# Kernel tuning notes

Measured on AMD Instinct MI355X. Metric: run time of the kernel, lower is better.

Reference implementation:

```python
import jax, jax.numpy as jnp
import numpy as np

G, N, F, H, E = 3, 40000, 256, 128, 640000


def gcn_conv(x, W, b, edge_index):
    """PyG GCNConv: x @ W, add self-loops, sym-normalized scatter-add, + bias."""
    n = x.shape[0]
    x = x @ W
    loop = jnp.arange(n)
    row = jnp.concatenate([edge_index[0], loop])  # source nodes
    col = jnp.concatenate([edge_index[1], loop])  # target nodes
    deg = jax.ops.segment_sum(jnp.ones_like(row, dtype=x.dtype), col, num_segments=n)
    dinv = jnp.where(deg > 0, jax.lax.rsqrt(jnp.maximum(deg, 1e-12)), 0.0)
    norm = dinv[row] * dinv[col]
    out = jax.ops.segment_sum(x[row] * norm[:, None], col, num_segments=n)
    return out + b


def setup_inputs() -> dict:
    key = jax.random.key(0)
    ks = jax.random.split(key, 14)
    inp = {
        'x': jax.random.normal(ks[0], (G, N, F), jnp.float32),
        'edge_index': jax.random.randint(ks[1], (G, 2, E), 0, N, jnp.int64),
        'fc1_W': jax.random.normal(ks[2], (G, F, H), jnp.float32) * 0.05,
        'fc1_b': jax.random.normal(ks[3], (G, H), jnp.float32) * 0.05,
        'conv1_W': jax.random.normal(ks[4], (G, H, H), jnp.float32) * 0.05,
        'conv1_b': jax.random.normal(ks[5], (G, H), jnp.float32) * 0.05,
        'conv2_W': jax.random.normal(ks[6], (G, H, H), jnp.float32) * 0.05,
        'conv2_b': jax.random.normal(ks[7], (G, H), jnp.float32) * 0.05,
        'dconv1_W': jax.random.normal(ks[8], (G, H, H), jnp.float32) * 0.05,
        'dconv1_b': jax.random.normal(ks[9], (G, H), jnp.float32) * 0.05,
        'dconv2_W': jax.random.normal(ks[10], (G, H, H), jnp.float32) * 0.05,
        'dconv2_b': jax.random.normal(ks[11], (G, H), jnp.float32) * 0.05,
        'fc2_W': jax.random.normal(ks[12], (H, F), jnp.float32) * 0.05,
        'fc2_b': jax.random.normal(ks[13], (F,), jnp.float32) * 0.05,
    }
    return inp


def reference(x, edge_index, fc1_W, fc1_b, conv1_W, conv1_b, conv2_W, conv2_b,
              dconv1_W, dconv1_b, dconv2_W, dconv2_b, fc2_W, fc2_b):
    def encoder(xi, ei, fw, fb, c1w, c1b, c2w, c2b):
        pre = xi @ fw + fb                     # fc1
        h = gcn_conv(pre, c1w, c1b, ei)
        h = gcn_conv(h, c2w, c2b, ei)
        return pre, jax.nn.relu(h)

    pre_feat, enc = jax.vmap(encoder)(x, edge_index, fc1_W, fc1_b,
                                      conv1_W, conv1_b, conv2_W, conv2_b)

    # Faithful reproduction of the sequentially-mutating cross-graph block.
    h = [enc[i] for i in range(G)]
    for i in range(G):
        for j in range(G):
            if j != i:
                h[i] = h[i] + h[j]
        h[i] = h[G - 1] - h[i]  # loop var j ends at G-1 (zeroes tensor when i==G-1)
        h[i] = gcn_conv(h[i], dconv1_W[i], dconv1_b[i], edge_index[i])
        h[i] = gcn_conv(h[i], dconv2_W[i], dconv2_b[i], edge_index[i])

    fin_feat = h[0]
    for k in range(1, G - 1):
        fin_feat = fin_feat + h[k]

    loss_embedding = jax.nn.softmax(fin_feat @ fc2_W + fc2_b, axis=-1)
    return pre_feat, enc, jnp.stack(h), fin_feat, loss_embedding
```

## Files before the change

kernel.cpp:

```cpp
#include <hip/hip_runtime.h>
#include <hip/hip_bf16.h>

#define NV 40000
#define FD 256
#define HD 128
#define ED 640000
#define NG 3
#define NH (NV*HD)

#define CH  64
#define EPC (ED/CH)
#define NB  625

typedef unsigned short u16;
typedef unsigned int   u32;
typedef __attribute__((ext_vector_type(8))) u16    u16x8;
typedef __attribute__((ext_vector_type(8))) __bf16 bf16x8;
typedef __attribute__((ext_vector_type(4))) float  f32x4;

__device__ inline u16 f2b(float f){ __bf16 h = (__bf16)f; return __builtin_bit_cast(u16, h); }
__device__ inline float b2f(u16 u){ u32 x = ((u32)u)<<16; return __builtin_bit_cast(float, x); }

__global__ __launch_bounds__(256) void histB_k(const int* __restrict__ ei, int* __restrict__ btot){
  int ch=blockIdx.x, g=blockIdx.y, t=threadIdx.x;
  __shared__ int h[NB];
  for (int i=t;i<NB;i+=256) h[i]=0;
  __syncthreads();
  const int* cc = ei + (long)g*2*ED + ED + ch*EPC;
  for (int j=t;j<EPC;j+=256) atomicAdd(&h[cc[j]>>6],1);
  __syncthreads();
  for (int b=t;b<NB;b+=256){ int v=h[b]; if(v) atomicAdd(&btot[g*NB+b], v); }
}

__global__ void scanB_k(const int* __restrict__ btot, int* __restrict__ base, int* __restrict__ gcur){
  __shared__ int wsum[16];
  int tid=threadIdx.x, lane=tid&63, wv=tid>>6;
  for (int g=0; g<NG; ++g){
    int v = (tid<NB)? btot[g*NB+tid] : 0;
    int s=v;
    #pragma unroll
    for (int d=1; d<64; d<<=1){ int u=__shfl_up(s,d,64); if(lane>=d) s+=u; }
    if (lane==63) wsum[wv]=s;
    __syncthreads();
    if (wv==0){
      int t3=(lane<16)?wsum[lane]:0;
      #pragma unroll
      for (int d=1; d<16; d<<=1){ int u=__shfl_up(t3,d,64); if(lane>=d) t3+=u; }
      if (lane<16) wsum[lane]=t3;
    }
    __syncthreads();
    int incl = s + (wv>0? wsum[wv-1]:0);
    if (tid<NB){
      base[g*(NB+1)+tid]=incl-v;
      gcur[g*NB+tid]=incl-v;
      if (tid==NB-1) base[g*(NB+1)+NB]=incl;
    }
    __syncthreads();
  }
}

__global__ __launch_bounds__(256) void scat_k(const int* __restrict__ ei, int* __restrict__ gcur,
                                              u32* __restrict__ temp){
  int ch=blockIdx.x, g=blockIdx.y, t=threadIdx.x;
  __shared__ int h[NB];
  __shared__ int cur[NB];
  for (int i=t;i<NB;i+=256) h[i]=0;
  __syncthreads();
  const int* rr = ei + (long)g*2*ED + ch*EPC;
  const int* cc = rr + ED;
  for (int j=t;j<EPC;j+=256) atomicAdd(&h[cc[j]>>6],1);
  __syncthreads();
  for (int b=t;b<NB;b+=256){ int v=h[b]; cur[b] = v? atomicAdd(&gcur[g*NB+b], v) : 0; }
  __syncthreads();
  u32* tg = temp + (long)g*ED;
  for (int j=t;j<EPC;j+=256){
    int r=rr[j], c=cc[j];
    int pos=atomicAdd(&cur[c>>6],1);
    tg[pos]=((u32)(c&63)<<16)|(u32)r;
  }
}

__global__ __launch_bounds__(256) void sort_k(const u32* __restrict__ temp, const int* __restrict__ base,
                                              u16* __restrict__ csr, int* __restrict__ cptr,
                                              float* __restrict__ dinv){
  int b=blockIdx.x, g=blockIdx.y, t=threadIdx.x;
  __shared__ int cnt[64];
  __shared__ int cur[64];
  if (t<64) cnt[t]=0;
  __syncthreads();
  const u32* tg = temp + (long)g*ED;
  int s=base[g*(NB+1)+b], e=base[g*(NB+1)+b+1];
  for (int i=s+t;i<e;i+=256) atomicAdd(&cnt[tg[i]>>16],1);
  __syncthreads();
  if (t<64){
    int v=cnt[t];
    int sc=v;
    #pragma unroll
    for (int d=1;d<64;d<<=1){ int u=__shfl_up(sc,d,64); if(t>=d) sc+=u; }
    int st = s + sc - v;
    cur[t]=st;
    cptr[(long)g*(NV+1) + b*64 + t] = st;
    if (b==NB-1 && t==63) cptr[(long)g*(NV+1)+NV] = e;
    dinv[(long)g*NV + b*64 + t] = rsqrtf((float)v+1.0f);
  }
  __syncthreads();
  u16* cg = csr + (long)g*ED;
  for (int i=s+t;i<e;i+=256){
    u32 tt=tg[i];
    int pos=atomicAdd(&cur[tt>>16],1);
    cg[pos]=(u16)(tt&0xFFFF);
  }
}

__global__ __launch_bounds__(256) void svec_k(const u16* __restrict__ csr, const int* __restrict__ cptr,
                                              const float* __restrict__ dinv, float* __restrict__ sv,
                                              int totWaves){
  int wid=(int)((blockIdx.x*256+threadIdx.x)>>6);
  if (wid>=totWaves) return;
  int lane=threadIdx.x&63;
  int g=wid/NV, c=wid-g*NV;
  const u16* cg=csr+(long)g*ED;
  const int* cp=cptr+(long)g*(NV+1);
  const float* dv=dinv+(long)g*NV;
  int j0=cp[c], j1=cp[c+1];
  float sum=0.f;
  for (int j=j0+lane;j<j1;j+=64) sum+=dv[cg[j]];
  #pragma unroll
  for (int o=32;o;o>>=1) sum+=__shfl_xor(sum,o,64);
  if (lane==0){ float dc=dv[c]; sv[(long)g*NV+c]=dc*(dc+sum); }
}

__device__ inline void tr_seg(const float* __restrict__ src, u16* __restrict__ dst,
                              int K, int NN, long idx, long total){
  if (idx>=total) return;
  long per=(long)K*NN; long mat=idx/per; long rem=idx-mat*per;
  int k=(int)(rem/NN), c=(int)(rem-(long)k*NN);
  dst[mat*per+(long)c*K+k]=f2b(src[idx]);
}

__global__ __launch_bounds__(256) void trall_k(
    const float* fc1W, const float* fc2W,
    const float* c1W, const float* c2W, const float* c1b,
    const float* d1W, const float* d2W, const float* d1b,
    u16* w_fc1, u16* w_fc2, u16* w_ce, u16* w_cd,
    float* t_enc, float* t_dec)
{
  int blk=blockIdx.x, t=threadIdx.x;
  if (blk < 384){
    tr_seg(fc1W, w_fc1, FD, HD, (long)blk*256+t, (long)NG*FD*HD);
  } else if (blk < 512){
    tr_seg(fc2W, w_fc2, HD, FD, (long)(blk-384)*256+t, (long)HD*FD);
  } else if (blk < 832){
    int bb=blk-512;
    int mat=bb>>6;
    int local=(bb&63)*256+t;
    int n=local>>7, k=local&127;
    const float* W1; const float* W2; u16* dst;
    if (mat<3){ W1=c1W+(long)mat*HD*HD; W2=c2W+(long)mat*HD*HD; dst=w_ce+(long)mat*HD*HD; }
    else { int md=mat-3; W1=d1W+(long)md*HD*HD; W2=d2W+(long)md*HD*HD; dst=w_cd+(long)md*HD*HD; }
    float s=0.f;
    for (int j=0;j<HD;j++) s += W1[k*HD+j]*W2[j*HD+n];
    dst[(long)n*HD+k]=f2b(s);
  } else {
    for (int idx=t; idx<768; idx+=256){
      int which=idx>>7, n=idx&127;
      const float* b; const float* W; float* dst;
      if (which<3){ b=c1b+which*HD; W=c2W+(long)which*HD*HD; dst=t_enc+which*HD; }
      else { int w2=which-3; b=d1b+w2*HD; W=d2W+(long)w2*HD*HD; dst=t_dec+w2*HD; }
      float s=0.f;
      for (int k=0;k<HD;k++) s += b[k]*W[(long)k*HD+n];
      dst[n]=s;
    }
  }
}

template<int MODE, int EX>
__global__ __launch_bounds__(256) void gemm_k(
    const void* __restrict__ A_, long sA,
    const u16* __restrict__ Bt, long sB,
    const float* __restrict__ biasCol, long sBias,
    const float* __restrict__ svec, long sS,
    const float* __restrict__ tvec,
    const float* __restrict__ scaleRow, long sSc,
    const float* __restrict__ Add,
    float* __restrict__ Cf, long sCf,
    float* __restrict__ Cf2,
    u16* __restrict__ Cb, long sCb,
    int M, int N, int K, int relu)
{
  __shared__ __align__(16) u16 lsA[128*64];
  __shared__ __align__(16) u16 lsB[128*64];
  const int gz = blockIdx.z;
  const float* Af = (const float*)A_ + (long)gz*sA;
  const u16*   Ab = (const u16*)  A_ + (long)gz*sA;
  const u16* Bp = Bt + (long)gz*sB;
  const int t = threadIdx.x;
  const int lane = t & 63, wv = t >> 6, wm = wv >> 1, wn = wv & 1;
  const int lr = lane & 15, lq = lane >> 4;
  const int ar = t >> 1, ah = t & 1;
  const long grow = (long)blockIdx.x*128 + ar;
  const int colB = blockIdx.y*128 + ar;

  f32x4 acc[4][4];
  #pragma unroll
  for (int m=0;m<4;m++)
    #pragma unroll
    for (int n=0;n<4;n++) acc[m][n] = (f32x4)(0.0f);

  for (int k0=0; k0<K; k0+=64){
    if (k0) __syncthreads();
    u16x8 av[4];
    if (grow < M){
      if (MODE==0){
        const u16x8* s = (const u16x8*)(Ab + grow*(long)K + k0 + ah*32);
        #pragma unroll
        for (int i=0;i<4;i++) av[i] = s[i];
      } else {
        const float4* s = (const float4*)(Af + grow*(long)K + k0 + ah*32);
        #pragma unroll
        for (int i=0;i<4;i++){
          float4 v0 = s[i*2], v1 = s[i*2+1];
          u16x8 w;
          w[0]=f2b(v0.x); w[1]=f2b(v0.y); w[2]=f2b(v0.z); w[3]=f2b(v0.w);
          w[4]=f2b(v1.x); w[5]=f2b(v1.y); w[6]=f2b(v1.z); w[7]=f2b(v1.w);
          av[i] = w;
        }
      }
    } else {
      #pragma unroll
      for (int i=0;i<4;i++) av[i] = (u16x8)((u16)0);
    }
    #pragma unroll
    for (int i=0;i<4;i++){
      int q = ah*4 + i;
      *(u16x8*)&lsA[ar*64 + ((q ^ (ar&7))<<3)] = av[i];
    }
    {
      const u16x8* s = (const u16x8*)(Bp + (long)colB*K + k0 + ah*32);
      #pragma unroll
      for (int i=0;i<4;i++){
        int q = ah*4 + i;
        *(u16x8*)&lsB[ar*64 + ((q ^ (ar&7))<<3)] = s[i];
      }
    }
    __syncthreads();
    #pragma unroll
    for (int kk=0; kk<2; kk++){
      bf16x8 afr[4], bfr[4];
      #pragma unroll
      for (int m=0;m<4;m++){
        int r = wm*64 + m*16 + lr;
        int q = kk*4 + lq;
        afr[m] = __builtin_bit_cast(bf16x8, *(const u16x8*)&lsA[r*64 + ((q ^ (r&7))<<3)]);
      }
      #pragma unroll
      for (int n=0;n<4;n++){
        int r = wn*64 + n*16 + lr;
        int q = kk*4 + lq;
        bfr[n] = __builtin_bit_cast(bf16x8, *(const u16x8*)&lsB[r*64 + ((q ^ (r&7))<<3)]);
      }
      #pragma unroll
      for (int m=0;m<4;m++)
        #pragma unroll
        for (int n=0;n<4;n++)
          acc[m][n] = __builtin_amdgcn_mfma_f32_16x16x32_bf16(afr[m], bfr[n], acc[m][n], 0, 0, 0);
    }
  }
  #pragma unroll
  for (int m=0;m<4;m++){
    long gr0 = (long)blockIdx.x*128 + wm*64 + m*16 + lq*4;
    #pragma unroll
    for (int n=0;n<4;n++){
      int gc = blockIdx.y*128 + wn*64 + n*16 + lr;
      float bb = biasCol[gz*sBias + gc];
      float tv = (svec!=nullptr) ? tvec[gz*sBias + gc] : 0.0f;
      #pragma unroll
      for (int i=0;i<4;i++){
        long gr = gr0 + i;
        if (gr < M){
          float v = acc[m][n][i] + bb;
          if (svec!=nullptr) v += svec[gz*sS + gr]*tv;
          if (relu) v = fmaxf(v, 0.0f);
          if (EX==0){
            if (Cf) Cf[gz*sCf + gr*(long)N + gc] = v;
            if (Cb){
              float sc = scaleRow ? scaleRow[gz*sSc + gr] : 1.0f;
              Cb[gz*sCb + gr*(long)N + gc] = f2b(v*sc);
            }
          } else if (EX==1){
            Cf[gz*sCf + gr*(long)N + gc] = v;
            float z = -(v + Add[gr*(long)N + gc]) * scaleRow[gr];
            Cb[gz*sCb + gr*(long)N + gc] = f2b(z);
          } else {
            Cf[gz*sCf + gr*(long)N + gc] = v;
            float fv = v + Add[gr*(long)N + gc];
            Cf2[gr*(long)N + gc] = fv;
            if (Cb) Cb[gz*sCb + gr*(long)N + gc] = f2b(fv);
          }
        }
      }
    }
  }
}

__global__ __launch_bounds__(256) void agg_k(
    const u16* __restrict__ xw, long sXW,
    const u16* __restrict__ csr, long sCsr,
    const int* __restrict__ cptr, long sCp,
    const float* __restrict__ dinv, long sD,
    u16* __restrict__ outB, long sOB,
    int totWaves, int scOut)
{
  int wid = (int)((blockIdx.x*256 + threadIdx.x) >> 6);
  if (wid >= totWaves) return;
  int lane = threadIdx.x & 63;
  int g = wid / NV;
  int c = wid - g*NV;
  const u32* xp = (const u32*)(xw + (long)g*sXW);
  const u16* cg = csr + (long)g*sCsr;
  const int* cp = cptr + (long)g*sCp;
  float dc = dinv[(long)g*sD + c];
  u32 u = xp[(c<<6) + lane];
  float sx = b2f((u16)u), sy = b2f((u16)(u>>16));
  int j0 = cp[c], j1 = cp[c+1];
  int deg = j1 - j0;
  int idx = 0;
  if (lane < deg) idx = cg[j0 + lane];
  int kmax = min(deg, 64);
  int k = 0;
  for (; k+8<=kmax; k+=8){
    int r0=__shfl(idx,k,64),   r1=__shfl(idx,k+1,64), r2=__shfl(idx,k+2,64), r3=__shfl(idx,k+3,64);
    int r4=__shfl(idx,k+4,64), r5=__shfl(idx,k+5,64), r6=__shfl(idx,k+6,64), r7=__shfl(idx,k+7,64);
    u32 v0=xp[(r0<<6)+lane], v1=xp[(r1<<6)+lane], v2=xp[(r2<<6)+lane], v3=xp[(r3<<6)+lane];
    u32 v4=xp[(r4<<6)+lane], v5=xp[(r5<<6)+lane], v6=xp[(r6<<6)+lane], v7=xp[(r7<<6)+lane];
    sx += b2f((u16)v0); sy += b2f((u16)(v0>>16));
    sx += b2f((u16)v1); sy += b2f((u16)(v1>>16));
    sx += b2f((u16)v2); sy += b2f((u16)(v2>>16));
    sx += b2f((u16)v3); sy += b2f((u16)(v3>>16));
    sx += b2f((u16)v4); sy += b2f((u16)(v4>>16));
    sx += b2f((u16)v5); sy += b2f((u16)(v5>>16));
    sx += b2f((u16)v6); sy += b2f((u16)(v6>>16));
    sx += b2f((u16)v7); sy += b2f((u16)(v7>>16));
  }
  for (; k+4<=kmax; k+=4){
    int r0=__shfl(idx,k,64), r1=__shfl(idx,k+1,64), r2=__shfl(idx,k+2,64), r3=__shfl(idx,k+3,64);
    u32 v0=xp[(r0<<6)+lane], v1=xp[(r1<<6)+lane], v2=xp[(r2<<6)+lane], v3=xp[(r3<<6)+lane];
    sx += b2f((u16)v0); sy += b2f((u16)(v0>>16));
    sx += b2f((u16)v1); sy += b2f((u16)(v1>>16));
    sx += b2f((u16)v2); sy += b2f((u16)(v2>>16));
    sx += b2f((u16)v3); sy += b2f((u16)(v3>>16));
  }
  for (; k<kmax; ++k){
    int r=__shfl(idx,k,64);
    u32 v=xp[(r<<6)+lane];
    sx += b2f((u16)v); sy += b2f((u16)(v>>16));
  }
  for (int j=j0+64; j<j1; ++j){
    int r=cg[j];
    u32 v=xp[(r<<6)+lane];
    sx += b2f((u16)v); sy += b2f((u16)(v>>16));
  }
  float m = scOut ? dc*dc : dc;
  float ox = m*sx, oy = m*sy;
  ((u32*)(outB + (long)g*sOB))[(c<<6) + lane] = (u32)f2b(ox) | ((u32)f2b(oy)<<16);
}

__global__ void ewzh2_k(const float4* __restrict__ e0, const float4* __restrict__ e1,
                        const float* __restrict__ dinv0, u16* __restrict__ outB,
                        const float* __restrict__ sv2, const float* __restrict__ t2,
                        const float* __restrict__ b2, float4* __restrict__ outH2){
  int blk = blockIdx.x;
  if (blk < (NH/4)/256){
    int i = blk*256 + threadIdx.x;
    int row = i>>5;
    float d = dinv0[row];
    float4 a = e0[i], b = e1[i];
    float x0=-d*(a.x+b.x), x1=-d*(a.y+b.y), x2=-d*(a.z+b.z), x3=-d*(a.w+b.w);
    ((uint2*)outB)[i] = make_uint2((u32)f2b(x0) | ((u32)f2b(x1)<<16),
                                   (u32)f2b(x2) | ((u32)f2b(x3)<<16));
  } else {
    int i = (blk - (NH/4)/256)*256 + threadIdx.x;
    int row = i>>5, c4 = i&31;
    float s = sv2[row];
    float4 tv = ((const float4*)t2)[c4];
    float4 bb = ((const float4*)b2)[c4];
    outH2[i] = make_float4(s*tv.x+bb.x, s*tv.y+bb.y, s*tv.z+bb.z, s*tv.w+bb.w);
  }
}

__global__ __launch_bounds__(256) void fc2sm_k(
    const u16* __restrict__ Ab, const u16* __restrict__ Bw,
    const float* __restrict__ bias, float* __restrict__ Out, int M)
{
  __shared__ __align__(16) u16 lsA[128*64];
  __shared__ __align__(16) u16 lsB[256*64];
  const int t = threadIdx.x;
  const int lane = t & 63, wv = t >> 6, wm = wv >> 1, wn = wv & 1;
  const int lr = lane & 15, lq = lane >> 4;
  const int ar = t >> 1, ah = t & 1;
  const long grow = (long)blockIdx.x*128 + ar;

  f32x4 acc[4][8];
  #pragma unroll
  for (int m=0;m<4;m++)
    #pragma unroll
    for (int n=0;n<8;n++) acc[m][n] = (f32x4)(0.0f);

  for (int k0=0; k0<128; k0+=64){
    if (k0) __syncthreads();
    {
      u16x8 av[4];
      if (grow < M){
        const u16x8* s = (const u16x8*)(Ab + grow*128L + k0 + ah*32);
        #pragma unroll
        for (int i=0;i<4;i++) av[i] = s[i];
      } else {
        #pragma unroll
        for (int i=0;i<4;i++) av[i] = (u16x8)((u16)0);
      }
      #pragma unroll
      for (int i=0;i<4;i++){
        int q = ah*4 + i;
        *(u16x8*)&lsA[ar*64 + ((q ^ (ar&7))<<3)] = av[i];
      }
    }
    #pragma unroll
    for (int rr=0; rr<2; rr++){
      int r = ar + rr*128;
      const u16x8* s = (const u16x8*)(Bw + (long)r*128 + k0 + ah*32);
      #pragma unroll
      for (int i=0;i<4;i++){
        int q = ah*4 + i;
        *(u16x8*)&lsB[r*64 + ((q ^ (r&7))<<3)] = s[i];
      }
    }
    __syncthreads();
    #pragma unroll
    for (int kk=0; kk<2; kk++){
      bf16x8 afr[4], bfr[8];
      #pragma unroll
      for (int m=0;m<4;m++){
        int r = wm*64 + m*16 + lr;
        int q = kk*4 + lq;
        afr[m] = __builtin_bit_cast(bf16x8, *(const u16x8*)&lsA[r*64 + ((q ^ (r&7))<<3)]);
      }
      #pragma unroll
      for (int n=0;n<8;n++){
        int r = wn*128 + n*16 + lr;
        int q = kk*4 + lq;
        bfr[n] = __builtin_bit_cast(bf16x8, *(const u16x8*)&lsB[r*64 + ((q ^ (r&7))<<3)]);
      }
      #pragma unroll
      for (int m=0;m<4;m++)
        #pragma unroll
        for (int n=0;n<8;n++)
          acc[m][n] = __builtin_amdgcn_mfma_f32_16x16x32_bf16(afr[m], bfr[n], acc[m][n], 0, 0, 0);
    }
  }
  #pragma unroll
  for (int n=0;n<8;n++){
    float bb = bias[wn*128 + n*16 + lr];
    #pragma unroll
    for (int m=0;m<4;m++)
      #pragma unroll
      for (int i=0;i<4;i++) acc[m][n][i] += bb;
  }
  __syncthreads();
  float* lsF = (float*)lsA;
  float pmax[4][4];
  #pragma unroll
  for (int m=0;m<4;m++)
    #pragma unroll
    for (int i=0;i<4;i++){
      float v = acc[m][0][i];
      #pragma unroll
      for (int n=1;n<8;n++) v = fmaxf(v, acc[m][n][i]);
      #pragma unroll
      for (int o=8;o;o>>=1) v = fmaxf(v, __shfl_xor(v, o, 16));
      pmax[m][i] = v;
      if (lr==0) lsF[(wm*64 + m*16 + lq*4 + i)*2 + wn] = v;
    }
  __syncthreads();
  float psum[4][4];
  #pragma unroll
  for (int m=0;m<4;m++)
    #pragma unroll
    for (int i=0;i<4;i++){
      int rl = wm*64 + m*16 + lq*4 + i;
      float rm = fmaxf(lsF[rl*2], lsF[rl*2+1]);
      float s = 0.f;
      #pragma unroll
      for (int n=0;n<8;n++){
        float e = __expf(acc[m][n][i] - rm);
        acc[m][n][i] = e;
        s += e;
      }
      #pragma unroll
      for (int o=8;o;o>>=1) s += __shfl_xor(s, o, 16);
      psum[m][i] = s;
      if (lr==0) lsF[256 + rl*2 + wn] = s;
    }
  __syncthreads();
  #pragma unroll
  for (int m=0;m<4;m++){
    long gr0 = (long)blockIdx.x*128 + wm*64 + m*16 + lq*4;
    #pragma unroll
    for (int i=0;i<4;i++){
      long gr = gr0 + i;
      if (gr < M){
        int rl = wm*64 + m*16 + lq*4 + i;
        float inv = 1.0f/(lsF[256 + rl*2] + lsF[256 + rl*2 + 1]);
        #pragma unroll
        for (int n=0;n<8;n++){
          int gc = wn*128 + n*16 + lr;
          Out[gr*256L + gc] = acc[m][n][i]*inv;
        }
      }
    }
  }
}

extern "C" void kernel_launch(void* const* d_in, const int* in_sizes, int n_in,
                              void* d_out, int out_size, void* d_ws, size_t ws_size,
                              hipStream_t stream)
{
  const float* x    = (const float*)d_in[0];
  const int*   ei   = (const int*)  d_in[1];
  const float* fc1W = (const float*)d_in[2];
  const float* fc1b = (const float*)d_in[3];
  const float* c1W  = (const float*)d_in[4];
  const float* c1b  = (const float*)d_in[5];
  const float* c2W  = (const float*)d_in[6];
  const float* c2b  = (const float*)d_in[7];
  const float* d1W  = (const float*)d_in[8];
  const float* d1b  = (const float*)d_in[9];
  const float* d2W  = (const float*)d_in[10];
  const float* d2b  = (const float*)d_in[11];
  const float* fc2W = (const float*)d_in[12];
  const float* fc2b = (const float*)d_in[13];
  (void)in_sizes; (void)n_in; (void)out_size; (void)ws_size;

  float* out  = (float*)d_out;
  float* O_pre = out;
  float* O_enc = out + (long)NG*NH;
  float* O_h   = out + 2L*NG*NH;
  float* O_fin = out + 3L*NG*NH;
  float* O_ls  = O_fin + NH;

  char* p = (char*)d_ws;
  auto alloc = [&](size_t bytes)->void*{
    void* r = (void*)p; p += (bytes + 255) & ~(size_t)255; return r;
  };
  u16* bfA    = (u16*)alloc((size_t)NG*NH*2);
  u16* bfB    = (u16*)alloc((size_t)NG*NH*2);
  u16* bfC    = (u16*)alloc((size_t)NG*NH*2);
  u16* wt_fc1 = (u16*)alloc((size_t)NG*FD*HD*2);
  u16* wt_fc2 = (u16*)alloc((size_t)HD*FD*2);
  u16* wt_ce  = (u16*)alloc((size_t)NG*HD*HD*2);
  u16* wt_cd  = (u16*)alloc((size_t)2*HD*HD*2);
  float* t_enc = (float*)alloc((size_t)NG*HD*4);
  float* t_dec = (float*)alloc((size_t)NG*HD*4);
  u32*  temp  = (u32*) alloc((size_t)NG*ED*4);
  u16*  csr   = (u16*) alloc((size_t)NG*ED*2);
  int*  cptr  = (int*) alloc((size_t)NG*(NV+1)*4);
  int*  btot  = (int*) alloc((size_t)NG*NB*4);
  int*  base  = (int*) alloc((size_t)NG*(NB+1)*4);
  int*  gcur  = (int*) alloc((size_t)NG*NB*4);
  float* dinv = (float*)alloc((size_t)NG*NV*4);
  float* svec = (float*)alloc((size_t)NG*NV*4);

  hipMemsetAsync(btot, 0, (size_t)NG*NB*4, stream);
  histB_k<<<dim3(CH,NG), 256, 0, stream>>>(ei, btot);
  scanB_k<<<1, 1024, 0, stream>>>(btot, base, gcur);
  scat_k<<<dim3(CH,NG), 256, 0, stream>>>(ei, gcur, temp);
  sort_k<<<dim3(NB,NG), 256, 0, stream>>>(temp, base, csr, cptr, dinv);
  svec_k<<<NG*NV/4, 256, 0, stream>>>(csr, cptr, dinv, svec, NG*NV);

  trall_k<<<833, 256, 0, stream>>>(fc1W, fc2W, c1W, c2W, c1b, d1W, d2W, d1b,
                                   wt_fc1, wt_fc2, wt_ce, wt_cd, t_enc, t_dec);

  dim3 g3((NV+127)/128, 1, NG);
  dim3 g1((NV+127)/128, 1, 1);

  gemm_k<1,0><<<g3, 256, 0, stream>>>(x, (long)NV*FD, wt_fc1, (long)FD*HD, fc1b, HD,
                                      nullptr, 0, nullptr, dinv, NV, nullptr,
                                      O_pre, NH, nullptr, bfA, NH, NV, HD, FD, 0);
  agg_k<<<NG*NV/4, 256, 0, stream>>>(bfA, NH, csr, ED, cptr, NV+1, dinv, NV, bfB, NH, NG*NV, 1);
  agg_k<<<NG*NV/4, 256, 0, stream>>>(bfB, NH, csr, ED, cptr, NV+1, dinv, NV, bfC, NH, NG*NV, 0);
  gemm_k<0,0><<<g3, 256, 0, stream>>>(bfC, NH, wt_ce, (long)HD*HD, c2b, HD,
                                      svec, NV, t_enc, nullptr, 0, nullptr,
                                      O_enc, NH, nullptr, nullptr, 0, NV, HD, HD, 1);

  ewzh2_k<<<2*(NH/4)/256, 256, 0, stream>>>((const float4*)O_enc, (const float4*)(O_enc+NH), dinv, bfA,
                                            svec + 2L*NV, t_dec + 2*HD, d2b + 2*HD,
                                            (float4*)(O_h + 2L*NH));

  agg_k<<<NV/4, 256, 0, stream>>>(bfA, 0, csr, 0, cptr, 0, dinv, 0, bfB, 0, NV, 1);
  agg_k<<<NV/4, 256, 0, stream>>>(bfB, 0, csr, 0, cptr, 0, dinv, 0, bfC, 0, NV, 0);
  gemm_k<0,1><<<g1, 256, 0, stream>>>(bfC, 0, wt_cd, 0, d2b, 0,
                                      svec, 0, t_dec, dinv + NV, 0, O_enc + NH,
                                      O_h, 0, nullptr, bfA, 0, NV, HD, HD, 0);

  agg_k<<<NV/4, 256, 0, stream>>>(bfA, 0, csr + (long)ED, 0, cptr + (NV+1), 0, dinv + NV, 0, bfB, 0, NV, 1);
  agg_k<<<NV/4, 256, 0, stream>>>(bfB, 0, csr + (long)ED, 0, cptr + (NV+1), 0, dinv + NV, 0, bfC, 0, NV, 0);
  gemm_k<0,2><<<g1, 256, 0, stream>>>(bfC, 0, wt_cd + (long)HD*HD, 0, d2b + HD, 0,
                                      svec + NV, 0, t_dec + HD, nullptr, 0, O_h,
                                      O_h + NH, 0, O_fin, bfA, 0, NV, HD, HD, 0);

  fc2sm_k<<<(NV+127)/128, 256, 0, stream>>>(bfA, wt_fc2, fc2b, O_ls, NV);
}
```

Baseline: 592.4 us.

## Merge histogram with weight prep, fuse svec into aggregation, rewrite agg with half-wave uint2 loads

Folds the edge histogram into the weight transpose/precompute kernel, and the per-node svec reduction into the first aggregation launch, to cut launches and let independent work share the GPU. The aggregation kernel now splits each wave into two halves that each handle a different neighbor and load 8-byte chunks of the row, combining the halves with a shuffle. The batched three-graph aggregation becomes per-graph launches, and unused softmax temporaries are dropped. This adds more kernel launches in the encoder stage and changes the reduction order in bf16 accumulation.

Result: slower. 605.7 us (+2.3%).

```diff
diff --git a/kernel.cpp b/kernel.cpp
--- a/kernel.cpp
+++ b/kernel.cpp
@@ -20,114 +20,9 @@
 
 __device__ inline u16 f2b(float f){ __bf16 h = (__bf16)f; return __builtin_bit_cast(u16, h); }
 __device__ inline float b2f(u16 u){ u32 x = ((u32)u)<<16; return __builtin_bit_cast(float, x); }
-
-__global__ __launch_bounds__(256) void histB_k(const int* __restrict__ ei, int* __restrict__ btot){
-  int ch=blockIdx.x, g=blockIdx.y, t=threadIdx.x;
-  __shared__ int h[NB];
-  for (int i=t;i<NB;i+=256) h[i]=0;
-  __syncthreads();
-  const int* cc = ei + (long)g*2*ED + ED + ch*EPC;
-  for (int j=t;j<EPC;j+=256) atomicAdd(&h[cc[j]>>6],1);
-  __syncthreads();
-  for (int b=t;b<NB;b+=256){ int v=h[b]; if(v) atomicAdd(&btot[g*NB+b], v); }
-}
-
-__global__ void scanB_k(const int* __restrict__ btot, int* __restrict__ base, int* __restrict__ gcur){
-  __shared__ int wsum[16];
-  int tid=threadIdx.x, lane=tid&63, wv=tid>>6;
-  for (int g=0; g<NG; ++g){
-    int v = (tid<NB)? btot[g*NB+tid] : 0;
-    int s=v;
-    #pragma unroll
-    for (int d=1; d<64; d<<=1){ int u=__shfl_up(s,d,64); if(lane>=d) s+=u; }
-    if (lane==63) wsum[wv]=s;
-    __syncthreads();
-    if (wv==0){
-      int t3=(lane<16)?wsum[lane]:0;
-      #pragma unroll
-      for (int d=1; d<16; d<<=1){ int u=__shfl_up(t3,d,64); if(lane>=d) t3+=u; }
-      if (lane<16) wsum[lane]=t3;
-    }
-    __syncthreads();
-    int incl = s + (wv>0? wsum[wv-1]:0);
-    if (tid<NB){
-      base[g*(NB+1)+tid]=incl-v;
-      gcur[g*NB+tid]=incl-v;
-      if (tid==NB-1) base[g*(NB+1)+NB]=incl;
-    }
-    __syncthreads();
-  }
-}
-
-__global__ __launch_bounds__(256) void scat_k(const int* __restrict__ ei, int* __restrict__ gcur,
-                                              u32* __restrict__ temp){
-  int ch=blockIdx.x, g=blockIdx.y, t=threadIdx.x;
-  __shared__ int h[NB];
-  __shared__ int cur[NB];
-  for (int i=t;i<NB;i+=256) h[i]=0;
-  __syncthreads();
-  const int* rr = ei + (long)g*2*ED + ch*EPC;
-  const int* cc = rr + ED;
-  for (int j=t;j<EPC;j+=256) atomicAdd(&h[cc[j]>>6],1);
-  __syncthreads();
-  for (int b=t;b<NB;b+=256){ int v=h[b]; cur[b] = v? atomicAdd(&gcur[g*NB+b], v) : 0; }
-  __syncthreads();
-  u32* tg = temp + (long)g*ED;
-  for (int j=t;j<EPC;j+=256){
-    int r=rr[j], c=cc[j];
-    int pos=atomicAdd(&cur[c>>6],1);
-    tg[pos]=((u32)(c&63)<<16)|(u32)r;
-  }
-}
-
-__global__ __launch_bounds__(256) void sort_k(const u32* __restrict__ temp, const int* __restrict__ base,
-                                              u16* __restrict__ csr, int* __restrict__ cptr,
-                                              float* __restrict__ dinv){
-  int b=blockIdx.x, g=blockIdx.y, t=threadIdx.x;
-  __shared__ int cnt[64];
-  __shared__ int cur[64];
-  if (t<64) cnt[t]=0;
-  __syncthreads();
-  const u32* tg = temp + (long)g*ED;
-  int s=base[g*(NB+1)+b], e=base[g*(NB+1)+b+1];
-  for (int i=s+t;i<e;i+=256) atomicAdd(&cnt[tg[i]>>16],1);
-  __syncthreads();
-  if (t<64){
-    int v=cnt[t];
-    int sc=v;
-    #pragma unroll
-    for (int d=1;d<64;d<<=1){ int u=__shfl_up(sc,d,64); if(t>=d) sc+=u; }
-    int st = s + sc - v;
-    cur[t]=st;
-    cptr[(long)g*(NV+1) + b*64 + t] = st;
-    if (b==NB-1 && t==63) cptr[(long)g*(NV+1)+NV] = e;
-    dinv[(long)g*NV + b*64 + t] = rsqrtf((float)v+1.0f);
-  }
-  __syncthreads();
-  u16* cg = csr + (long)g*ED;
-  for (int i=s+t;i<e;i+=256){
-    u32 tt=tg[i];
-    int pos=atomicAdd(&cur[tt>>16],1);
-    cg[pos]=(u16)(tt&0xFFFF);
-  }
-}
-
-__global__ __launch_bounds__(256) void svec_k(const u16* __restrict__ csr, const int* __restrict__ cptr,
-                                              const float* __restrict__ dinv, float* __restrict__ sv,
-                                              int totWaves){
-  int wid=(int)((blockIdx.x*256+threadIdx.x)>>6);
-  if (wid>=totWaves) return;
-  int lane=threadIdx.x&63;
-  int g=wid/NV, c=wid-g*NV;
-  const u16* cg=csr+(long)g*ED;
-  const int* cp=cptr+(long)g*(NV+1);
-  const float* dv=dinv+(long)g*NV;
-  int j0=cp[c], j1=cp[c+1];
-  float sum=0.f;
-  for (int j=j0+lane;j<j1;j+=64) sum+=dv[cg[j]];
-  #pragma unroll
-  for (int o=32;o;o>>=1) sum+=__shfl_xor(sum,o,64);
-  if (lane==0){ float dc=dv[c]; sv[(long)g*NV+c]=dc*(dc+sum); }
+__device__ inline void acc2(u32 w, float&a, float&b){
+  a += __builtin_bit_cast(float, w<<16);
+  b += __builtin_bit_cast(float, w & 0xFFFF0000u);
 }
 
 __device__ inline void tr_seg(const float* __restrict__ src, u16* __restrict__ dst,
@@ -138,14 +33,27 @@
   dst[mat*per+(long)c*K+k]=f2b(src[idx]);
 }
 
-__global__ __launch_bounds__(256) void trall_k(
+__global__ __launch_bounds__(256) void htr_k(
+    const int* __restrict__ ei, int* __restrict__ btot,
     const float* fc1W, const float* fc2W,
     const float* c1W, const float* c2W, const float* c1b,
     const float* d1W, const float* d2W, const float* d1b,
     u16* w_fc1, u16* w_fc2, u16* w_ce, u16* w_cd,
     float* t_enc, float* t_dec)
 {
-  int blk=blockIdx.x, t=threadIdx.x;
+  __shared__ int h[NB];
+  int b = blockIdx.x, t = threadIdx.x;
+  if (b < 192){
+    int ch = b % CH, g = b / CH;
+    for (int i=t;i<NB;i+=256) h[i]=0;
+    __syncthreads();
+    const int* cc = ei + (long)g*2*ED + ED + ch*EPC;
+    for (int j=t;j<EPC;j+=256) atomicAdd(&h[cc[j]>>6],1);
+    __syncthreads();
+    for (int bb=t;bb<NB;bb+=256){ int v=h[bb]; if(v) atomicAdd(&btot[g*NB+bb], v); }
+    return;
+  }
+  int blk = b - 192;
   if (blk < 384){
     tr_seg(fc1W, w_fc1, FD, HD, (long)blk*256+t, (long)NG*FD*HD);
   } else if (blk < 512){
@@ -164,13 +72,195 @@
   } else {
     for (int idx=t; idx<768; idx+=256){
       int which=idx>>7, n=idx&127;
-      const float* b; const float* W; float* dst;
-      if (which<3){ b=c1b+which*HD; W=c2W+(long)which*HD*HD; dst=t_enc+which*HD; }
-      else { int w2=which-3; b=d1b+w2*HD; W=d2W+(long)w2*HD*HD; dst=t_dec+w2*HD; }
+      const float* bv; const float* W; float* dst;
+      if (which<3){ bv=c1b+which*HD; W=c2W+(long)which*HD*HD; dst=t_enc+which*HD; }
+      else { int w2=which-3; bv=d1b+w2*HD; W=d2W+(long)w2*HD*HD; dst=t_dec+w2*HD; }
       float s=0.f;
-      for (int k=0;k<HD;k++) s += b[k]*W[(long)k*HD+n];
+      for (int k=0;k<HD;k++) s += bv[k]*W[(long)k*HD+n];
       dst[n]=s;
     }
+  }
+}
+
+__global__ void scanB_k(const int* __restrict__ btot, int* __restrict__ base, int* __restrict__ gcur){
+  __shared__ int wsum[16];
+  int tid=threadIdx.x, lane=tid&63, wv=tid>>6;
+  for (int g=0; g<NG; ++g){
+    int v = (tid<NB)? btot[g*NB+tid] : 0;
+    int s=v;
+    #pragma unroll
+    for (int d=1; d<64; d<<=1){ int u=__shfl_up(s,d,64); if(lane>=d) s+=u; }
+    if (lane==63) wsum[wv]=s;
+    __syncthreads();
+    if (wv==0){
+      int t3=(lane<16)?wsum[lane]:0;
+      #pragma unroll
+      for (int d=1; d<16; d<<=1){ int u=__shfl_up(t3,d,64); if(lane>=d) t3+=u; }
+      if (lane<16) wsum[lane]=t3;
+    }
+    __syncthreads();
+    int incl = s + (wv>0? wsum[wv-1]:0);
+    if (tid<NB){
+      base[g*(NB+1)+tid]=incl-v;
+      gcur[g*NB+tid]=incl-v;
+      if (tid==NB-1) base[g*(NB+1)+NB]=incl;
+    }
+    __syncthreads();
+  }
+}
+
+__global__ __launch_bounds__(256) void scat_k(const int* __restrict__ ei, int* __restrict__ gcur,
+                                              u32* __restrict__ temp){
+  int ch=blockIdx.x, g=blockIdx.y, t=threadIdx.x;
+  __shared__ int h[NB];
+  __shared__ int cur[NB];
+  for (int i=t;i<NB;i+=256) h[i]=0;
+  __syncthreads();
+  const int* rr = ei + (long)g*2*ED + ch*EPC;
+  const int* cc = rr + ED;
+  for (int j=t;j<EPC;j+=256) atomicAdd(&h[cc[j]>>6],1);
+  __syncthreads();
+  for (int b=t;b<NB;b+=256){ int v=h[b]; cur[b] = v? atomicAdd(&gcur[g*NB+b], v) : 0; }
+  __syncthreads();
+  u32* tg = temp + (long)g*ED;
+  for (int j=t;j<EPC;j+=256){
+    int r=rr[j], c=cc[j];
+    int pos=atomicAdd(&cur[c>>6],1);
+    tg[pos]=((u32)(c&63)<<16)|(u32)r;
+  }
+}
+
+__global__ __launch_bounds__(256) void sort_k(const u32* __restrict__ temp, const int* __restrict__ base,
+                                              u16* __restrict__ csr, int* __restrict__ cptr,
+                                              float* __restrict__ dinv){
+  int b=blockIdx.x, g=blockIdx.y, t=threadIdx.x;
+  __shared__ int cnt[64];
+  __shared__ int cur[64];
+  if (t<64) cnt[t]=0;
+  __syncthreads();
+  const u32* tg = temp + (long)g*ED;
+  int s=base[g*(NB+1)+b], e=base[g*(NB+1)+b+1];
+  for (int i=s+t;i<e;i+=256) atomicAdd(&cnt[tg[i]>>16],1);
+  __syncthreads();
+  if (t<64){
+    int v=cnt[t];
+    int sc=v;
+    #pragma unroll
+    for (int d=1;d<64;d<<=1){ int u=__shfl_up(sc,d,64); if(t>=d) sc+=u; }
+    int st = s + sc - v;
+    cur[t]=st;
+    cptr[(long)g*(NV+1) + b*64 + t] = st;
+    if (b==NB-1 && t==63) cptr[(long)g*(NV+1)+NV] = e;
+    dinv[(long)g*NV + b*64 + t] = rsqrtf((float)v+1.0f);
+  }
+  __syncthreads();
+  u16* cg = csr + (long)g*ED;
+  for (int i=s+t;i<e;i+=256){
+    u32 tt=tg[i];
+    int pos=atomicAdd(&cur[tt>>16],1);
+    cg[pos]=(u16)(tt&0xFFFF);
+  }
+}
+
+__device__ __forceinline__ void agg_body(
+    const u16* __restrict__ xw, const u16* __restrict__ csr,
+    const int* __restrict__ cptr, const float* __restrict__ dinv,
+    u16* __restrict__ outB, int c, int lane, int scOut)
+{
+  const uint2* xp2 = (const uint2*)xw;
+  int hl = lane & 31;
+  int hi = lane >> 5;
+  float dc = dinv[c];
+  float s0=0.f, s1=0.f, s2=0.f, s3=0.f;
+  {
+    uint2 v = xp2[(long)c*32 + hl];
+    if (hi==0){ acc2(v.x, s0, s1); acc2(v.y, s2, s3); }
+  }
+  int j0 = cptr[c], j1 = cptr[c+1];
+  int deg = j1 - j0;
+  int idx = 0;
+  if (lane < deg) idx = csr[j0 + lane];
+  int nhc = min((deg+1)>>1, 32);
+  int i = 0;
+  for (; 2*i+7 < deg && i+4 <= nhc; i+=4){
+    int p0=__shfl(idx, 2*i+hi,   64);
+    int p1=__shfl(idx, 2*i+2+hi, 64);
+    int p2=__shfl(idx, 2*i+4+hi, 64);
+    int p3=__shfl(idx, 2*i+6+hi, 64);
+    uint2 v0=xp2[(long)p0*32+hl], v1=xp2[(long)p1*32+hl];
+    uint2 v2=xp2[(long)p2*32+hl], v3=xp2[(long)p3*32+hl];
+    acc2(v0.x,s0,s1); acc2(v0.y,s2,s3);
+    acc2(v1.x,s0,s1); acc2(v1.y,s2,s3);
+    acc2(v2.x,s0,s1); acc2(v2.y,s2,s3);
+    acc2(v3.x,s0,s1); acc2(v3.y,s2,s3);
+  }
+  for (; i<nhc; ++i){
+    int e = 2*i+hi;
+    int p = __shfl(idx, e<deg ? e : 0, 64);
+    if (e < deg){
+      uint2 v=xp2[(long)p*32+hl];
+      acc2(v.x,s0,s1); acc2(v.y,s2,s3);
+    }
+  }
+  if (deg > 64){
+    int nt = deg - 64;
+    int nth = (nt - hi + 1) >> 1;
+    for (int i2=0; i2<nth; ++i2){
+      int r = csr[j0 + 64 + 2*i2 + hi];
+      uint2 v = xp2[(long)r*32+hl];
+      acc2(v.x,s0,s1); acc2(v.y,s2,s3);
+    }
+  }
+  s0 += __shfl_xor(s0,32,64);
+  s1 += __shfl_xor(s1,32,64);
+  s2 += __shfl_xor(s2,32,64);
+  s3 += __shfl_xor(s3,32,64);
+  if (hi==0){
+    float m = scOut ? dc*dc : dc;
+    u32 lo  = (u32)f2b(m*s0) | ((u32)f2b(m*s1)<<16);
+    u32 hi2 = (u32)f2b(m*s2) | ((u32)f2b(m*s3)<<16);
+    ((uint2*)outB)[(long)c*32 + hl] = make_uint2(lo, hi2);
+  }
+}
+
+__device__ __forceinline__ void svec_body(
+    const u16* __restrict__ csr, const int* __restrict__ cptr,
+    const float* __restrict__ dinv, float* __restrict__ sv, int wid, int lane)
+{
+  int g = wid / NV, c = wid - g*NV;
+  const u16* cg = csr + (long)g*ED;
+  const int* cp = cptr + (long)g*(NV+1);
+  const float* dv = dinv + (long)g*NV;
+  int j0=cp[c], j1=cp[c+1];
+  float sum=0.f;
+  for (int j=j0+lane;j<j1;j+=64) sum+=dv[cg[j]];
+  #pragma unroll
+  for (int o=32;o;o>>=1) sum+=__shfl_xor(sum,o,64);
+  if (lane==0){ float dc=dv[c]; sv[(long)g*NV+c]=dc*(dc+sum); }
+}
+
+__global__ __launch_bounds__(256) void agg_k(
+    const u16* __restrict__ xw, const u16* __restrict__ csr,
+    const int* __restrict__ cptr, const float* __restrict__ dinv,
+    u16* __restrict__ outB, int scOut)
+{
+  int wid = (int)((blockIdx.x*256 + threadIdx.x) >> 6);
+  agg_body(xw, csr, cptr, dinv, outB, wid, threadIdx.x & 63, scOut);
+}
+
+__global__ __launch_bounds__(256) void aggsv_k(
+    const u16* __restrict__ xw, const u16* __restrict__ csr,
+    const int* __restrict__ cptr, const float* __restrict__ dinv,
+    u16* __restrict__ outB, int scOut,
+    const u16* __restrict__ csrA, const int* __restrict__ cptrA,
+    const float* __restrict__ dinvA, float* __restrict__ sv)
+{
+  if (blockIdx.x < NV/4){
+    int wid = (int)((blockIdx.x*256 + threadIdx.x) >> 6);
+    agg_body(xw, csr, cptr, dinv, outB, wid, threadIdx.x & 63, scOut);
+  } else {
+    int wid = (int)(((blockIdx.x - NV/4)*256 + threadIdx.x) >> 6);
+    svec_body(csrA, cptrA, dinvA, sv, wid, threadIdx.x & 63);
   }
 }
 
@@ -303,68 +393,6 @@
   }
 }
 
-__global__ __launch_bounds__(256) void agg_k(
-    const u16* __restrict__ xw, long sXW,
-    const u16* __restrict__ csr, long sCsr,
-    const int* __restrict__ cptr, long sCp,
-    const float* __restrict__ dinv, long sD,
-    u16* __restrict__ outB, long sOB,
-    int totWaves, int scOut)
-{
-  int wid = (int)((blockIdx.x*256 + threadIdx.x) >> 6);
-  if (wid >= totWaves) return;
-  int lane = threadIdx.x & 63;
-  int g = wid / NV;
-  int c = wid - g*NV;
-  const u32* xp = (const u32*)(xw + (long)g*sXW);
-  const u16* cg = csr + (long)g*sCsr;
-  const int* cp = cptr + (long)g*sCp;
-  float dc = dinv[(long)g*sD + c];
-  u32 u = xp[(c<<6) + lane];
-  float sx = b2f((u16)u), sy = b2f((u16)(u>>16));
-  int j0 = cp[c], j1 = cp[c+1];
-  int deg = j1 - j0;
-  int idx = 0;
-  if (lane < deg) idx = cg[j0 + lane];
-  int kmax = min(deg, 64);
-  int k = 0;
-  for (; k+8<=kmax; k+=8){
-    int r0=__shfl(idx,k,64),   r1=__shfl(idx,k+1,64), r2=__shfl(idx,k+2,64), r3=__shfl(idx,k+3,64);
-    int r4=__shfl(idx,k+4,64), r5=__shfl(idx,k+5,64), r6=__shfl(idx,k+6,64), r7=__shfl(idx,k+7,64);
-    u32 v0=xp[(r0<<6)+lane], v1=xp[(r1<<6)+lane], v2=xp[(r2<<6)+lane], v3=xp[(r3<<6)+lane];
-    u32 v4=xp[(r4<<6)+lane], v5=xp[(r5<<6)+lane], v6=xp[(r6<<6)+lane], v7=xp[(r7<<6)+lane];
-    sx += b2f((u16)v0); sy += b2f((u16)(v0>>16));
-    sx += b2f((u16)v1); sy += b2f((u16)(v1>>16));
-    sx += b2f((u16)v2); sy += b2f((u16)(v2>>16));
-    sx += b2f((u16)v3); sy += b2f((u16)(v3>>16));
-    sx += b2f((u16)v4); sy += b2f((u16)(v4>>16));
-    sx += b2f((u16)v5); sy += b2f((u16)(v5>>16));
-    sx += b2f((u16)v6); sy += b2f((u16)(v6>>16));
-    sx += b2f((u16)v7); sy += b2f((u16)(v7>>16));
-  }
-  for (; k+4<=kmax; k+=4){
-    int r0=__shfl(idx,k,64), r1=__shfl(idx,k+1,64), r2=__shfl(idx,k+2,64), r3=__shfl(idx,k+3,64);
-    u32 v0=xp[(r0<<6)+lane], v1=xp[(r1<<6)+lane], v2=xp[(r2<<6)+lane], v3=xp[(r3<<6)+lane];
-    sx += b2f((u16)v0); sy += b2f((u16)(v0>>16));
-    sx += b2f((u16)v1); sy += b2f((u16)(v1>>16));
-    sx += b2f((u16)v2); sy += b2f((u16)(v2>>16));
-    sx += b2f((u16)v3); sy += b2f((u16)(v3>>16));
-  }
-  for (; k<kmax; ++k){
-    int r=__shfl(idx,k,64);
-    u32 v=xp[(r<<6)+lane];
-    sx += b2f((u16)v); sy += b2f((u16)(v>>16));
-  }
-  for (int j=j0+64; j<j1; ++j){
-    int r=cg[j];
-    u32 v=xp[(r<<6)+lane];
-    sx += b2f((u16)v); sy += b2f((u16)(v>>16));
-  }
-  float m = scOut ? dc*dc : dc;
-  float ox = m*sx, oy = m*sy;
-  ((u32*)(outB + (long)g*sOB))[(c<<6) + lane] = (u32)f2b(ox) | ((u32)f2b(oy)<<16);
-}
-
 __global__ void ewzh2_k(const float4* __restrict__ e0, const float4* __restrict__ e1,
                         const float* __restrict__ dinv0, u16* __restrict__ outB,
                         const float* __restrict__ sv2, const float* __restrict__ t2,
@@ -467,7 +495,6 @@
   }
   __syncthreads();
   float* lsF = (float*)lsA;
-  float pmax[4][4];
   #pragma unroll
   for (int m=0;m<4;m++)
     #pragma unroll
@@ -477,11 +504,9 @@
       for (int n=1;n<8;n++) v = fmaxf(v, acc[m][n][i]);
       #pragma unroll
       for (int o=8;o;o>>=1) v = fmaxf(v, __shfl_xor(v, o, 16));
-      pmax[m][i] = v;
       if (lr==0) lsF[(wm*64 + m*16 + lq*4 + i)*2 + wn] = v;
     }
   __syncthreads();
-  float psum[4][4];
   #pragma unroll
   for (int m=0;m<4;m++)
     #pragma unroll
@@ -497,7 +522,6 @@
       }
       #pragma unroll
       for (int o=8;o;o>>=1) s += __shfl_xor(s, o, 16);
-      psum[m][i] = s;
       if (lr==0) lsF[256 + rl*2 + wn] = s;
     }
   __syncthreads();
@@ -570,14 +594,11 @@
   float* svec = (float*)alloc((size_t)NG*NV*4);
 
   hipMemsetAsync(btot, 0, (size_t)NG*NB*4, stream);
-  histB_k<<<dim3(CH,NG), 256, 0, stream>>>(ei, btot);
+  htr_k<<<192+833, 256, 0, stream>>>(ei, btot, fc1W, fc2W, c1W, c2W, c1b, d1W, d2W, d1b,
+                                     wt_fc1, wt_fc2, wt_ce, wt_cd, t_enc, t_dec);
   scanB_k<<<1, 1024, 0, stream>>>(btot, base, gcur);
   scat_k<<<dim3(CH,NG), 256, 0, stream>>>(ei, gcur, temp);
   sort_k<<<dim3(NB,NG), 256, 0, stream>>>(temp, base, csr, cptr, dinv);
-  svec_k<<<NG*NV/4, 256, 0, stream>>>(csr, cptr, dinv, svec, NG*NV);
-
-  trall_k<<<833, 256, 0, stream>>>(fc1W, fc2W, c1W, c2W, c1b, d1W, d2W, d1b,
-                                   wt_fc1, wt_fc2, wt_ce, wt_cd, t_enc, t_dec);
 
   dim3 g3((NV+127)/128, 1, NG);
   dim3 g1((NV+127)/128, 1, 1);
@@ -585,8 +606,15 @@
   gemm_k<1,0><<<g3, 256, 0, stream>>>(x, (long)NV*FD, wt_fc1, (long)FD*HD, fc1b, HD,
                                       nullptr, 0, nullptr, dinv, NV, nullptr,
                                       O_pre, NH, nullptr, bfA, NH, NV, HD, FD, 0);
-  agg_k<<<NG*NV/4, 256, 0, stream>>>(bfA, NH, csr, ED, cptr, NV+1, dinv, NV, bfB, NH, NG*NV, 1);
-  agg_k<<<NG*NV/4, 256, 0, stream>>>(bfB, NH, csr, ED, cptr, NV+1, dinv, NV, bfC, NH, NG*NV, 0);
+
+  aggsv_k<<<NV/4 + 3*NV/4, 256, 0, stream>>>(bfA, csr, cptr, dinv, bfB, 1,
+                                             csr, cptr, dinv, svec);
+  agg_k<<<NV/4, 256, 0, stream>>>(bfA + NH,   csr + ED,   cptr + (NV+1),   dinv + NV,   bfB + NH,   1);
+  agg_k<<<NV/4, 256, 0, stream>>>(bfA + 2L*NH, csr + 2L*ED, cptr + 2*(NV+1), dinv + 2L*NV, bfB + 2L*NH, 1);
+  agg_k<<<NV/4, 256, 0, stream>>>(bfB,        csr,        cptr,            dinv,        bfC,        0);
+  agg_k<<<NV/4, 256, 0, stream>>>(bfB + NH,   csr + ED,   cptr + (NV+1),   dinv + NV,   bfC + NH,   0);
+  agg_k<<<NV/4, 256, 0, stream>>>(bfB + 2L*NH, csr + 2L*ED, cptr + 2*(NV+1), dinv + 2L*NV, bfC + 2L*NH, 0);
+
   gemm_k<0,0><<<g3, 256, 0, stream>>>(bfC, NH, wt_ce, (long)HD*HD, c2b, HD,
                                       svec, NV, t_enc, nullptr, 0, nullptr,
                                       O_enc, NH, nullptr, nullptr, 0, NV, HD, HD, 1);
@@ -595,14 +623,14 @@
                                             svec + 2L*NV, t_dec + 2*HD, d2b + 2*HD,
                                             (float4*)(O_h + 2L*NH));
 
-  agg_k<<<NV/4, 256, 0, stream>>>(bfA, 0, csr, 0, cptr, 0, dinv, 0, bfB, 0, NV, 1);
-  agg_k<<<NV/4, 256, 0, stream>>>(bfB, 0, csr, 0, cptr, 0, dinv, 0, bfC, 0, NV, 0);
+  agg_k<<<NV/4, 256, 0, stream>>>(bfA, csr, cptr, dinv, bfB, 1);
+  agg_k<<<NV/4, 256, 0, stream>>>(bfB, csr, cptr, dinv, bfC, 0);
   gemm_k<0,1><<<g1, 256, 0, stream>>>(bfC, 0, wt_cd, 0, d2b, 0,
                                       svec, 0, t_dec, dinv + NV, 0, O_enc + NH,
                                       O_h, 0, nullptr, bfA, 0, NV, HD, HD, 0);
 
-  agg_k<<<NV/4, 256, 0, stream>>>(bfA, 0, csr + (long)ED, 0, cptr + (NV+1), 0, dinv + NV, 0, bfB, 0, NV, 1);
-  agg_k<<<NV/4, 256, 0, stream>>>(bfB, 0, csr + (long)ED, 0, cptr + (NV+1), 0, dinv + NV, 0, bfC, 0, NV, 0);
+  agg_k<<<NV/4, 256, 0, stream>>>(bfA, csr + ED, cptr + (NV+1), dinv + NV, bfB, 1);
+  agg_k<<<NV/4, 256, 0, stream>>>(bfB, csr + ED, cptr + (NV+1), dinv + NV, bfC, 0);
   gemm_k<0,2><<<g1, 256, 0, stream>>>(bfC, 0, wt_cd + (long)HD*HD, 0, d2b + HD, 0,
                                       svec + NV, 0, t_dec + HD, nullptr, 0, O_h,
                                       O_h + NH, 0, O_fin, bfA, 0, NV, HD, HD, 0);
```
